# Performance work log

Measured on AMD Instinct MI355X. Metric: run time of the kernel, lower is better.

## Reference

```python
import jax, jax.numpy as jnp
import numpy as np

MASK_NUM = -2.0 ** 32 + 1.0  # additive mask value from the module


def setup_inputs() -> dict:
    key = jax.random.key(0)
    k1, k2, k3, k4 = jax.random.split(key, 4)
    BH, S, D = 32, 2048, 64   # batch*heads, seq, head_dim
    B = 2                      # true batch for key padding masks
    q = jax.random.normal(k1, (BH, S, D), dtype=jnp.float32)
    k = jax.random.normal(k2, (BH, S, D), dtype=jnp.float32)
    v = jax.random.normal(k3, (BH, S, D), dtype=jnp.float32)
    masks = jax.random.randint(k4, (B, S), 0, 2, dtype=jnp.int32)  # 1 = masked key
    return {"q": q, "k": k, "v": v, "masks": masks}


def reference(q, k, v, masks):
    # scores: [BH, Sq, Sk]
    d = q.shape[-1]
    scores = jnp.einsum("bqd,bkd->bqk", q, k) / jnp.sqrt(jnp.float32(d))
    # tile key-padding masks over heads: [B,Sk] -> [BH,Sk], add big negative
    tile = q.shape[0] // masks.shape[0]
    m = jnp.tile(masks.astype(jnp.float32), (tile, 1))  # [BH, Sk]
    scores = scores + m[:, None, :] * MASK_NUM
    attn = jax.nn.softmax(scores, axis=-1)
    # dropout rate is 0.0 -> identity
    out = jnp.einsum("bqk,bkd->bqd", attn, v)
    return out
```

## Files before the change

### kernel.cpp

```cpp
#include <hip/hip_runtime.h>
#include <hip/hip_bf16.h>


#define SQ 2048
#define DD 64
#define NT 32

typedef __attribute__((ext_vector_type(8)))  short bf16x8;
typedef __attribute__((ext_vector_type(16))) float f32x16;
typedef __attribute__((ext_vector_type(2)))  unsigned uint2v;

#define LOG2E  1.4426950408889634f
#define QSCALE (0.125f * LOG2E)
#define MASKV  (-4294967295.0f * LOG2E)
#define FM     20.0f

__device__ __forceinline__ int cvt_pk(float lo, float hi) {
    int r;
    asm("v_cvt_pk_bf16_f32 %0, %1, %2" : "=v"(r) : "v"(lo), "v"(hi));
    return r;
}
__device__ __forceinline__ int koff(int c, int e) {
    return c * 1024 + ((e ^ (((c & 3) << 1) | (e >> 5))) << 4);
}
__device__ __forceinline__ void plswap2(unsigned a, unsigned b,
                                        unsigned& lo01, unsigned& hi23, int hi) {
#if __has_builtin(__builtin_amdgcn_permlane32_swap)
    uint2v r = __builtin_amdgcn_permlane32_swap(a, b, false, false);
    lo01 = r[0]; hi23 = r[1];
#else
    unsigned pa = (unsigned)__shfl_xor((int)a, 32);
    unsigned pb = (unsigned)__shfl_xor((int)b, 32);
    lo01 = hi ? pb : a;
    hi23 = hi ? b : pa;
#endif
}

__global__ __launch_bounds__(256, 2) void attn_fwd(
    const float* __restrict__ q, const float* __restrict__ k,
    const float* __restrict__ v, const int* __restrict__ masks,
    float* __restrict__ out)
{
    __shared__ alignas(16) char smem[32768];

    const int x    = blockIdx.x;
    const int orig = (x & 7) * 64 + (x >> 3);
    const int h    = orig >> 4;
    const int qb   = orig & 15;
    const int tid  = threadIdx.x;
    const int w    = tid >> 6;
    const int lane = tid & 63;
    const int l31  = lane & 31;
    const int hi   = lane >> 5;

    const float* __restrict__ qh = q + (size_t)h * SQ * DD;
    const float* __restrict__ kh = k + (size_t)h * SQ * DD;
    const float* __restrict__ vh = v + (size_t)h * SQ * DD;
    const int*   __restrict__ mrow = masks + (h & 1) * SQ;

    const int qrow = qb * 128 + w * 32 + l31;
    bf16x8 qf[4];
#pragma unroll
    for (int dc = 0; dc < 4; ++dc) {
        const float* p = qh + (size_t)qrow * DD + dc * 16 + hi * 8;
        float4 a = *(const float4*)p;
        float4 b = *(const float4*)(p + 4);
        union { int i[4]; bf16x8 v; } f;
        f.i[0] = cvt_pk(a.x * QSCALE, a.y * QSCALE);
        f.i[1] = cvt_pk(a.z * QSCALE, a.w * QSCALE);
        f.i[2] = cvt_pk(b.x * QSCALE, b.y * QSCALE);
        f.i[3] = cvt_pk(b.z * QSCALE, b.w * QSCALE);
        qf[dc] = f.v;
    }

    union { int i[4]; bf16x8 v; } onesu;
    onesu.i[0] = onesu.i[1] = onesu.i[2] = onesu.i[3] = 0x3f803f80;
    const bf16x8 ones = onesu.v;

    f32x16 o[2], lacc;
#pragma unroll
    for (int dt = 0; dt < 2; ++dt)
#pragma unroll
      for (int i = 0; i < 16; ++i) o[dt][i] = 0.f;
#pragma unroll
    for (int i = 0; i < 16; ++i) lacc[i] = 0.f;

    const int rK = tid >> 3, cK = tid & 7;
    const int aV = tid & 31, dV = (tid >> 5) * 8;
    const int eK = ((cK & 1) << 5) | rK;
    const int kA_off = koff(cK >> 1,       eK);
    const int kB_off = koff(4 + (cK >> 1), eK);

    float4 kA0, kA1, kB0, kB1, vA0, vA1, vB0, vB1;
    int4 mxa[4], mxb[4], mya[4], myb[4];

#define LOADKV(kt)                                                        \
    {   const float* kpA = kh + (size_t)((kt) + rK) * DD + 8 * cK;       \
        const float* kpB = kpA + 32 * DD;                                 \
        const float* vpA = vh + (size_t)((kt) + 2 * aV) * DD + dV;       \
        const float* vpB = vpA + DD;                                      \
        kA0 = *(const float4*)kpA; kA1 = *(const float4*)(kpA + 4);      \
        kB0 = *(const float4*)kpB; kB1 = *(const float4*)(kpB + 4);      \
        vA0 = *(const float4*)vpA; vA1 = *(const float4*)(vpA + 4);      \
        vB0 = *(const float4*)vpB; vB1 = *(const float4*)(vpB + 4);      }

#define LOADM(kt, Ma, Mb)                                                 \
    {   const int* mk_ = mrow + (kt) + 4 * hi;                            \
        Ma[0] = *(const int4*)(mk_);      Ma[1] = *(const int4*)(mk_ + 8);  \
        Ma[2] = *(const int4*)(mk_ + 16); Ma[3] = *(const int4*)(mk_ + 24); \
        Mb[0] = *(const int4*)(mk_ + 32); Mb[1] = *(const int4*)(mk_ + 40); \
        Mb[2] = *(const int4*)(mk_ + 48); Mb[3] = *(const int4*)(mk_ + 56); }

#define WRITEK(Kp)                                                        \
    {   union { int i[4]; bf16x8 b; } kw;                                 \
        kw.i[0] = cvt_pk(kA0.x, kA0.y); kw.i[1] = cvt_pk(kA0.z, kA0.w);  \
        kw.i[2] = cvt_pk(kA1.x, kA1.y); kw.i[3] = cvt_pk(kA1.z, kA1.w);  \
        *(bf16x8*)((Kp) + kA_off) = kw.b;                                 \
        kw.i[0] = cvt_pk(kB0.x, kB0.y); kw.i[1] = cvt_pk(kB0.z, kB0.w);  \
        kw.i[2] = cvt_pk(kB1.x, kB1.y); kw.i[3] = cvt_pk(kB1.z, kB1.w);  \
        *(bf16x8*)((Kp) + kB_off) = kw.b;                                 }

#define WRITEV(Vp)                                                        \
    {   float va[8] = {vA0.x, vA0.y, vA0.z, vA0.w, vA1.x, vA1.y, vA1.z, vA1.w}; \
        float vb[8] = {vB0.x, vB0.y, vB0.z, vB0.w, vB1.x, vB1.y, vB1.z, vB1.w}; \
        _Pragma("unroll")                                                 \
        for (int j = 0; j < 8; ++j) {                                     \
            const int r_ = dV + j;                                        \
            const int cv_ = ((aV >> 3) << 1) | (r_ >> 5);                 \
            const int ev_ = (((aV >> 2) & 1) << 5) | (r_ & 31);           \
            *(unsigned*)((Vp) + koff(cv_, ev_) + 4 * (aV & 3))            \
                = (unsigned)cvt_pk(va[j], vb[j]);                         \
        }                                                                 }

#define TILE(KT, KbP, VbP, KnP, VnP, MCa, MCb, MNa, MNb, MORE)            \
    {   const bool more_ = (MORE);                                        \
        if (more_) { LOADKV((KT) + 64) LOADM((KT) + 64, MNa, MNb) }      \
        __builtin_amdgcn_sched_barrier(0);                                \
        f32x16 s0, s1;                                                    \
        _Pragma("unroll")                                                 \
        for (int g = 0; g < 4; ++g) {                                     \
            s0[4*g+0] = MCa[g].x ? MASKV : 0.f;                           \
            s0[4*g+1] = MCa[g].y ? MASKV : 0.f;                           \
            s0[4*g+2] = MCa[g].z ? MASKV : 0.f;                           \
            s0[4*g+3] = MCa[g].w ? MASKV : 0.f;                           \
            s1[4*g+0] = MCb[g].x ? MASKV : 0.f;                           \
            s1[4*g+1] = MCb[g].y ? MASKV : 0.f;                           \
            s1[4*g+2] = MCb[g].z ? MASKV : 0.f;                           \
            s1[4*g+3] = MCb[g].w ? MASKV : 0.f;                           \
        }                                                                 \
        __builtin_amdgcn_s_setprio(1);                                    \
        _Pragma("unroll")                                                 \
        for (int dc = 0; dc < 4; ++dc) {                                  \
            bf16x8 k0 = *(const bf16x8*)((KbP) + koff(dc,     lane));     \
            bf16x8 k1 = *(const bf16x8*)((KbP) + koff(4 + dc, lane));     \
            s0 = __builtin_amdgcn_mfma_f32_32x32x16_bf16(k0, qf[dc], s0, 0, 0, 0); \
            s1 = __builtin_amdgcn_mfma_f32_32x32x16_bf16(k1, qf[dc], s1, 0, 0, 0); \
        }                                                                 \
        __builtin_amdgcn_s_setprio(0);                                    \
        _Pragma("unroll")                                                 \
        for (int i = 0; i < 16; ++i) {                                    \
            s0[i] = __builtin_amdgcn_exp2f(s0[i] - FM);                   \
            s1[i] = __builtin_amdgcn_exp2f(s1[i] - FM);                   \
        }                                                                 \
        unsigned pk[2][4][2];                                             \
        _Pragma("unroll")                                                 \
        for (int g = 0; g < 4; ++g) {                                     \
            pk[0][g][0] = (unsigned)cvt_pk(s0[4*g+0], s0[4*g+1]);         \
            pk[0][g][1] = (unsigned)cvt_pk(s0[4*g+2], s0[4*g+3]);         \
            pk[1][g][0] = (unsigned)cvt_pk(s1[4*g+0], s1[4*g+1]);         \
            pk[1][g][1] = (unsigned)cvt_pk(s1[4*g+2], s1[4*g+3]);         \
        }                                                                 \
        __builtin_amdgcn_s_setprio(1);                                    \
        _Pragma("unroll")                                                 \
        for (int kc = 0; kc < 4; ++kc) {                                  \
            const int kb = kc >> 1, kp = kc & 1;                          \
            union { unsigned u[4]; bf16x8 b; } pu;                        \
            unsigned lo0, hi0, lo1, hi1;                                  \
            plswap2(pk[kb][2*kp][0], pk[kb][2*kp+1][0], lo0, hi0, hi);    \
            plswap2(pk[kb][2*kp][1], pk[kb][2*kp+1][1], lo1, hi1, hi);    \
            pu.u[0] = lo0; pu.u[1] = lo1; pu.u[2] = hi0; pu.u[3] = hi1;   \
            _Pragma("unroll")                                             \
            for (int dt = 0; dt < 2; ++dt) {                              \
                bf16x8 vf = *(const bf16x8*)((VbP) + koff(kc * 2 + dt, lane)); \
                o[dt] = __builtin_amdgcn_mfma_f32_32x32x16_bf16(vf, pu.b, o[dt], 0, 0, 0); \
            }                                                             \
            lacc = __builtin_amdgcn_mfma_f32_32x32x16_bf16(ones, pu.b, lacc, 0, 0, 0); \
        }                                                                 \
        __builtin_amdgcn_s_setprio(0);                                    \
        if (more_) { WRITEK(KnP) WRITEV(VnP) }                            \
        __syncthreads();                                                  \
    }

    LOADKV(0)
    LOADM(0, mxa, mxb)
    WRITEK(smem)
    WRITEV(smem + 8192)
    __syncthreads();

    char* const b0K = smem;
    char* const b0V = smem + 8192;
    char* const b1K = smem + 16384;
    char* const b1V = smem + 24576;

    for (int it2 = 0; it2 < NT / 2; ++it2) {
        const int kt0 = it2 * 128;
        TILE(kt0,      b0K, b0V, b1K, b1V, mxa, mxb, mya, myb, true)
        TILE(kt0 + 64, b1K, b1V, b0K, b0V, mya, myb, mxa, mxb, it2 + 1 < NT / 2)
    }

    const float invl = 1.0f / lacc[0];
    float* op = out + (size_t)h * SQ * DD + (size_t)qrow * DD;
#pragma unroll
    for (int dt = 0; dt < 2; ++dt)
#pragma unroll
      for (int g = 0; g < 4; ++g) {
        float4 r = { o[dt][4*g+0] * invl, o[dt][4*g+1] * invl,
                     o[dt][4*g+2] * invl, o[dt][4*g+3] * invl };
        *(float4*)(op + 32 * dt + 8 * g + 4 * hi) = r;
      }
}

extern "C" void kernel_launch(void* const* d_in, const int* in_sizes, int n_in,
                              void* d_out, int out_size, void* d_ws, size_t ws_size,
                              hipStream_t stream) {
    const float* q = (const float*)d_in[0];
    const float* k = (const float*)d_in[1];
    const float* v = (const float*)d_in[2];
    const int* masks = (const int*)d_in[3];
    float* out = (float*)d_out;
    attn_fwd<<<dim3(512), dim3(256), 0, stream>>>(q, k, v, masks, out);
}
```

Before: 77.91 us.

## Prefetch K/V global loads two tiles ahead with double register staging

```diff
diff --git a/kernel.cpp b/kernel.cpp
--- a/kernel.cpp
+++ b/kernel.cpp
@@ -36,6 +36,8 @@
 #endif
 }
 
+struct Stage { float4 kA0, kA1, kB0, kB1, vA0, vA1, vB0, vB1; };
+
 __global__ __launch_bounds__(256, 2) void attn_fwd(
     const float* __restrict__ q, const float* __restrict__ k,
     const float* __restrict__ v, const int* __restrict__ masks,
@@ -91,18 +93,18 @@
     const int kA_off = koff(cK >> 1,       eK);
     const int kB_off = koff(4 + (cK >> 1), eK);
 
-    float4 kA0, kA1, kB0, kB1, vA0, vA1, vB0, vB1;
+    Stage sA, sB;
     int4 mxa[4], mxb[4], mya[4], myb[4];
 
-#define LOADKV(kt)                                                        \
+#define LOADKV(kt, S)                                                     \
     {   const float* kpA = kh + (size_t)((kt) + rK) * DD + 8 * cK;       \
         const float* kpB = kpA + 32 * DD;                                 \
         const float* vpA = vh + (size_t)((kt) + 2 * aV) * DD + dV;       \
         const float* vpB = vpA + DD;                                      \
-        kA0 = *(const float4*)kpA; kA1 = *(const float4*)(kpA + 4);      \
-        kB0 = *(const float4*)kpB; kB1 = *(const float4*)(kpB + 4);      \
-        vA0 = *(const float4*)vpA; vA1 = *(const float4*)(vpA + 4);      \
-        vB0 = *(const float4*)vpB; vB1 = *(const float4*)(vpB + 4);      }
+        S.kA0 = *(const float4*)kpA; S.kA1 = *(const float4*)(kpA + 4);  \
+        S.kB0 = *(const float4*)kpB; S.kB1 = *(const float4*)(kpB + 4);  \
+        S.vA0 = *(const float4*)vpA; S.vA1 = *(const float4*)(vpA + 4);  \
+        S.vB0 = *(const float4*)vpB; S.vB1 = *(const float4*)(vpB + 4);  }
 
 #define LOADM(kt, Ma, Mb)                                                 \
     {   const int* mk_ = mrow + (kt) + 4 * hi;                            \
@@ -111,18 +113,20 @@
         Mb[0] = *(const int4*)(mk_ + 32); Mb[1] = *(const int4*)(mk_ + 40); \
         Mb[2] = *(const int4*)(mk_ + 48); Mb[3] = *(const int4*)(mk_ + 56); }
 
-#define WRITEK(Kp)                                                        \
+#define WRITEK(Kp, S)                                                     \
     {   union { int i[4]; bf16x8 b; } kw;                                 \
-        kw.i[0] = cvt_pk(kA0.x, kA0.y); kw.i[1] = cvt_pk(kA0.z, kA0.w);  \
-        kw.i[2] = cvt_pk(kA1.x, kA1.y); kw.i[3] = cvt_pk(kA1.z, kA1.w);  \
+        kw.i[0] = cvt_pk(S.kA0.x, S.kA0.y); kw.i[1] = cvt_pk(S.kA0.z, S.kA0.w); \
+        kw.i[2] = cvt_pk(S.kA1.x, S.kA1.y); kw.i[3] = cvt_pk(S.kA1.z, S.kA1.w); \
         *(bf16x8*)((Kp) + kA_off) = kw.b;                                 \
-        kw.i[0] = cvt_pk(kB0.x, kB0.y); kw.i[1] = cvt_pk(kB0.z, kB0.w);  \
-        kw.i[2] = cvt_pk(kB1.x, kB1.y); kw.i[3] = cvt_pk(kB1.z, kB1.w);  \
+        kw.i[0] = cvt_pk(S.kB0.x, S.kB0.y); kw.i[1] = cvt_pk(S.kB0.z, S.kB0.w); \
+        kw.i[2] = cvt_pk(S.kB1.x, S.kB1.y); kw.i[3] = cvt_pk(S.kB1.z, S.kB1.w); \
         *(bf16x8*)((Kp) + kB_off) = kw.b;                                 }
 
-#define WRITEV(Vp)                                                        \
-    {   float va[8] = {vA0.x, vA0.y, vA0.z, vA0.w, vA1.x, vA1.y, vA1.z, vA1.w}; \
-        float vb[8] = {vB0.x, vB0.y, vB0.z, vB0.w, vB1.x, vB1.y, vB1.z, vB1.w}; \
+#define WRITEV(Vp, S)                                                     \
+    {   float va[8] = {S.vA0.x, S.vA0.y, S.vA0.z, S.vA0.w,               \
+                       S.vA1.x, S.vA1.y, S.vA1.z, S.vA1.w};              \
+        float vb[8] = {S.vB0.x, S.vB0.y, S.vB0.z, S.vB0.w,               \
+                       S.vB1.x, S.vB1.y, S.vB1.z, S.vB1.w};              \
         _Pragma("unroll")                                                 \
         for (int j = 0; j < 8; ++j) {                                     \
             const int r_ = dV + j;                                        \
@@ -132,9 +136,9 @@
                 = (unsigned)cvt_pk(va[j], vb[j]);                         \
         }                                                                 }
 
-#define TILE(KT, KbP, VbP, KnP, VnP, MCa, MCb, MNa, MNb, MORE)            \
-    {   const bool more_ = (MORE);                                        \
-        if (more_) { LOADKV((KT) + 64) LOADM((KT) + 64, MNa, MNb) }      \
+#define TILE(KT, KbP, VbP, KnP, VnP, MCa, MCb, MNa, MNb, SL, SW, DOL, DOM, DOW) \
+    {   if (DOL) LOADKV((KT) + 128, SL)                                   \
+        if (DOM) LOADM((KT) + 64, MNa, MNb)                               \
         __builtin_amdgcn_sched_barrier(0);                                \
         f32x16 s0, s1;                                                    \
         _Pragma("unroll")                                                 \
@@ -187,25 +191,29 @@
             lacc = __builtin_amdgcn_mfma_f32_32x32x16_bf16(ones, pu.b, lacc, 0, 0, 0); \
         }                                                                 \
         __builtin_amdgcn_s_setprio(0);                                    \
-        if (more_) { WRITEK(KnP) WRITEV(VnP) }                            \
+        if (DOW) { WRITEK(KnP, SW) WRITEV(VnP, SW) }                      \
         __syncthreads();                                                  \
     }
-
-    LOADKV(0)
-    LOADM(0, mxa, mxb)
-    WRITEK(smem)
-    WRITEV(smem + 8192)
-    __syncthreads();
 
     char* const b0K = smem;
     char* const b0V = smem + 8192;
     char* const b1K = smem + 16384;
     char* const b1V = smem + 24576;
 
+    LOADKV(0, sA)
+    LOADM(0, mxa, mxb)
+    WRITEK(b0K, sA)
+    WRITEV(b0V, sA)
+    LOADKV(64, sB)
+    __syncthreads();
+
     for (int it2 = 0; it2 < NT / 2; ++it2) {
         const int kt0 = it2 * 128;
-        TILE(kt0,      b0K, b0V, b1K, b1V, mxa, mxb, mya, myb, true)
-        TILE(kt0 + 64, b1K, b1V, b0K, b0V, mya, myb, mxa, mxb, it2 + 1 < NT / 2)
+        const bool morePair = (kt0 + 128 < SQ);
+        TILE(kt0, b0K, b0V, b1K, b1V, mxa, mxb, mya, myb, sA, sB,
+             morePair, true, true)
+        TILE(kt0 + 64, b1K, b1V, b0K, b0V, mya, myb, mxa, mxb, sB, sA,
+             (kt0 + 192 < SQ), morePair, morePair)
     }
 
     const float invl = 1.0f / lacc[0];
```

Measured after the change: 77.37 us. Within noise of the previous version (-0.7%).
